# Kernel tuning notes

Hardware: AMD Instinct MI355X
Metric: run time of the kernel (lower is better)

## Reference

```python
import jax, jax.numpy as jnp
import numpy as np

N_VAR = 1_000_000
N_CON = 500_000
N_EDGE = 8_000_000
H = 10  # n_h_feats


def setup_inputs() -> dict:
    key = jax.random.key(0)
    ks = jax.random.split(key, 20)
    f32 = jnp.float32
    s = 0.3  # weight init scale
    return {
        'var_c': jax.random.normal(ks[0], (N_VAR,), f32),
        'var_x': jax.random.normal(ks[1], (N_VAR,), f32),
        'con_b': jax.random.normal(ks[2], (N_CON,), f32),
        'edge_src': jax.random.randint(ks[3], (N_EDGE,), 0, N_VAR, jnp.int32),
        'edge_dst': jax.random.randint(ks[4], (N_EDGE,), 0, N_CON, jnp.int32),
        'edge_w': jax.random.uniform(ks[5], (N_EDGE,), f32),
        'Wv': jax.random.normal(ks[6], (2, H), f32) * s,
        'bv': jnp.zeros((H,), f32),
        'Wc': jax.random.normal(ks[7], (1, H), f32) * s,
        'bc': jnp.zeros((H,), f32),
        'W1': jax.random.normal(ks[8], (H, H), f32) * s,
        'b1': jnp.zeros((H,), f32),
        'W2': jax.random.normal(ks[9], (H, H), f32) * s,
        'b2': jnp.zeros((H,), f32),
        'Wo1': jax.random.normal(ks[10], (H, H), f32) * s,
        'bo1': jnp.zeros((H,), f32),
        'Wo2': jax.random.normal(ks[11], (H, H), f32) * s,
        'bo2': jnp.zeros((H,), f32),
        'Wo3': jax.random.normal(ks[12], (H, 1), f32) * s,
        'bo3': jnp.zeros((1,), f32),
    }


def _graph_conv(feat_src, src, dst, w, n_dst, deg_src, deg_dst, W, b):
    # DGL GraphConv, norm='both', with edge weights:
    # h = D_src^{-1/2} x ; m_e = h[src_e] * w_e ; agg = scatter_sum(m, dst)
    # out = (D_dst^{-1/2} agg) @ W + b
    h = feat_src * jax.lax.rsqrt(deg_src)[:, None]
    m = h[src] * w[:, None]                      # [E, H] gather + scale
    agg = jax.ops.segment_sum(m, dst, num_segments=n_dst)  # scatter-add
    agg = agg * jax.lax.rsqrt(deg_dst)[:, None]
    return agg @ W + b


def reference(var_c, var_x, con_b, edge_src, edge_dst, edge_w,
              Wv, bv, Wc, bc, W1, b1, W2, b2, Wo1, bo1, Wo2, bo2, Wo3, bo3):
    # node embeddings
    var_feat = jnp.stack([var_c, var_x], axis=1)            # [N_VAR, 2]
    con_feat = con_b.reshape(-1, 1)                          # [N_CON, 1]
    X_var = jax.nn.relu(var_feat @ Wv + bv)                  # [N_VAR, H]
    X_con = jax.nn.relu(con_feat @ Wc + bc)                  # computed in original; unused by GraphConv (no dst-feat term)

    ones_e = jnp.ones((edge_src.shape[0],), jnp.float32)
    deg_var = jnp.maximum(jax.ops.segment_sum(ones_e, edge_src, num_segments=N_VAR), 1.0)
    deg_con = jnp.maximum(jax.ops.segment_sum(ones_e, edge_dst, num_segments=N_CON), 1.0)

    # conv1['con'] is overwritten by conv2['con'] in the original (v2c src feats are X_var both times)
    h_con = jax.nn.relu(_graph_conv(X_var, edge_src, edge_dst, edge_w, N_CON, deg_var, deg_con, W2, b2))
    # likewise conv1['var'] is overwritten by conv2['var'] (c2v src feats are h_con both times)
    h_var = jax.nn.relu(_graph_conv(h_con, edge_dst, edge_src, edge_w, N_VAR, deg_con, deg_var, W2, b2))

    z = jax.nn.relu(h_var @ Wo1 + bo1)
    z = jax.nn.relu(z @ Wo2 + bo2)
    logit = z @ Wo3 + bo3                                    # [N_VAR, 1]
    # dgl.readout_nodes(op='mean') over a single batched graph
    return jnp.mean(logit, axis=0, keepdims=True)            # [1, 1]
```

## Files before the change

kernel.cpp:

```cpp
#include <hip/hip_runtime.h>

#define NVAR 1000000
#define NCON 500000
#define EPB 8192
#define FCAP 4480


__global__ __launch_bounds__(256) void kA_hist2(const int4* __restrict__ src4,
                                                const int4* __restrict__ dst4,
                                                unsigned* __restrict__ bhV,
                                                unsigned* __restrict__ bhC,
                                                int ne4, int nblk) {
    __shared__ unsigned hv[1024], hc[1024];
    int tid = threadIdx.x, b = blockIdx.x;
    for (int t = tid; t < 1024; t += 256) { hv[t] = 0; hc[t] = 0; }
    __syncthreads();
    int beg = b * (EPB / 4), end = min(ne4, beg + (EPB / 4));
    for (int i = beg + tid; i < end; i += 256) {
        int4 s = src4[i];
        int4 d = dst4[i];
        atomicAdd(&hv[s.x >> 10], 1u); atomicAdd(&hv[s.y >> 10], 1u);
        atomicAdd(&hv[s.z >> 10], 1u); atomicAdd(&hv[s.w >> 10], 1u);
        atomicAdd(&hc[d.x >> 9], 1u);  atomicAdd(&hc[d.y >> 9], 1u);
        atomicAdd(&hc[d.z >> 9], 1u);  atomicAdd(&hc[d.w >> 9], 1u);
    }
    __syncthreads();
    for (int t = tid; t < 1024; t += 256) {
        bhV[(size_t)t * nblk + b] = hv[t];
        bhC[(size_t)t * nblk + b] = hc[t];
    }
}

__global__ __launch_bounds__(256) void kA_scat(const int* __restrict__ keys,
                                               const int* __restrict__ vals,
                                               const float* __restrict__ w,
                                               const unsigned int* __restrict__ scanned,
                                               int2* __restrict__ bucketed,
                                               int ne, int shift, int nblk) {
    __shared__ unsigned int h[1024];
    __shared__ unsigned int lb[1024];
    __shared__ unsigned int gb[1024];
    __shared__ unsigned int sc[256];
    __shared__ int2 stage[EPB];
    __shared__ unsigned short sbkt[EPB];
    int tid = threadIdx.x, b = blockIdx.x;
    for (int t = tid; t < 1024; t += 256) {
        h[t] = 0;
        gb[t] = scanned[(size_t)t * nblk + b];
    }
    __syncthreads();
    int beg = b * EPB, end = min(ne, beg + EPB), cnt = end - beg;
    int cnt4 = cnt >> 2;
    const int4* keys4 = (const int4*)(keys + beg);
    for (int i = tid; i < cnt4; i += 256) {
        int4 k = keys4[i];
        atomicAdd(&h[k.x >> shift], 1u);
        atomicAdd(&h[k.y >> shift], 1u);
        atomicAdd(&h[k.z >> shift], 1u);
        atomicAdd(&h[k.w >> shift], 1u);
    }
    for (int i = cnt4 * 4 + tid; i < cnt; i += 256) atomicAdd(&h[keys[beg + i] >> shift], 1u);
    __syncthreads();
    unsigned v0, v1, v2, v3;
    int q = tid * 4;
    v0 = h[q]; v1 = h[q + 1]; v2 = h[q + 2]; v3 = h[q + 3];
    sc[tid] = v0 + v1 + v2 + v3;
    __syncthreads();
    for (int dd = 1; dd < 256; dd <<= 1) {
        unsigned add = (tid >= dd) ? sc[tid - dd] : 0u;
        __syncthreads();
        sc[tid] += add;
        __syncthreads();
    }
    unsigned ex = (tid == 0) ? 0u : sc[tid - 1];
    lb[q]     = ex;
    lb[q + 1] = ex + v0;
    lb[q + 2] = ex + v0 + v1;
    lb[q + 3] = ex + v0 + v1 + v2;
    __syncthreads();
    for (int t = tid; t < 1024; t += 256) h[t] = 0;
    __syncthreads();
    unsigned mask = (1u << shift) - 1u;
    const int4* vals4 = (const int4*)(vals + beg);
    const float4* w4 = (const float4*)(w + beg);
    for (int i = tid; i < cnt4; i += 256) {
        int4 k = keys4[i];
        int4 v = vals4[i];
        float4 ww = w4[i];
        {
            unsigned bkt = (unsigned)k.x >> shift;
            unsigned r = atomicAdd(&h[bkt], 1u);
            unsigned slot = lb[bkt] + r;
            stage[slot] = make_int2(__float_as_int(ww.x),
                                    (v.x << shift) | (unsigned)(k.x & (int)mask));
            sbkt[slot] = (unsigned short)bkt;
        }
        {
            unsigned bkt = (unsigned)k.y >> shift;
            unsigned r = atomicAdd(&h[bkt], 1u);
            unsigned slot = lb[bkt] + r;
            stage[slot] = make_int2(__float_as_int(ww.y),
                                    (v.y << shift) | (unsigned)(k.y & (int)mask));
            sbkt[slot] = (unsigned short)bkt;
        }
        {
            unsigned bkt = (unsigned)k.z >> shift;
            unsigned r = atomicAdd(&h[bkt], 1u);
            unsigned slot = lb[bkt] + r;
            stage[slot] = make_int2(__float_as_int(ww.z),
                                    (v.z << shift) | (unsigned)(k.z & (int)mask));
            sbkt[slot] = (unsigned short)bkt;
        }
        {
            unsigned bkt = (unsigned)k.w >> shift;
            unsigned r = atomicAdd(&h[bkt], 1u);
            unsigned slot = lb[bkt] + r;
            stage[slot] = make_int2(__float_as_int(ww.w),
                                    (v.w << shift) | (unsigned)(k.w & (int)mask));
            sbkt[slot] = (unsigned short)bkt;
        }
    }
    for (int i = cnt4 * 4 + tid; i < cnt; i += 256) {
        int k = keys[beg + i];
        unsigned bkt = (unsigned)k >> shift;
        unsigned r = atomicAdd(&h[bkt], 1u);
        unsigned slot = lb[bkt] + r;
        stage[slot] = make_int2(__float_as_int(w[beg + i]),
                                (vals[beg + i] << shift) | (unsigned)(k & (int)mask));
        sbkt[slot] = (unsigned short)bkt;
    }
    __syncthreads();
    for (int i = tid; i < cnt; i += 256) {
        unsigned bb = sbkt[i];
        bucketed[gb[bb] + ((unsigned)i - lb[bb])] = stage[i];
    }
}

__global__ __launch_bounds__(256) void kDeg(const int2* __restrict__ bucketed,
                                            const unsigned* __restrict__ scanned,
                                            unsigned* __restrict__ deg,
                                            int nnodes, int nblk, int lowbits) {
    __shared__ unsigned h[1024];
    int d = blockIdx.x, tid = threadIdx.x;
    int W = 1 << lowbits;
    unsigned mask = (unsigned)(W - 1);
    unsigned base = scanned[(size_t)d * nblk], next = scanned[(size_t)(d + 1) * nblk];
    for (int t = tid; t < W; t += 256) h[t] = 0;
    __syncthreads();
    for (unsigned i = base + tid; i < next; i += 256)
        atomicAdd(&h[(unsigned)bucketed[i].y & mask], 1u);
    __syncthreads();
    int lo = d << lowbits;
    for (int t = tid; t < W; t += 256) {
        int node = lo + t;
        if (node < nnodes) deg[node] = h[t];
    }
}

__global__ __launch_bounds__(256) void kDegPackV(const int2* __restrict__ bucketed,
                                                 const unsigned* __restrict__ scanned,
                                                 const float* __restrict__ var_c,
                                                 const float* __restrict__ var_x,
                                                 unsigned* __restrict__ deg,
                                                 float4* __restrict__ vcr,
                                                 int nnodes, int nblk) {
    __shared__ unsigned h[1024];
    int d = blockIdx.x, tid = threadIdx.x;
    unsigned base = scanned[(size_t)d * nblk], next = scanned[(size_t)(d + 1) * nblk];
    for (int t = tid; t < 1024; t += 256) h[t] = 0;
    __syncthreads();
    for (unsigned i = base + tid; i < next; i += 256)
        atomicAdd(&h[(unsigned)bucketed[i].y & 1023u], 1u);
    __syncthreads();
    int lo = d << 10;
    for (int t = tid; t < 1024; t += 256) {
        int node = lo + t;
        if (node < nnodes) {
            unsigned dg = h[t];
            deg[node] = dg;
            float rs = rsqrtf(fmaxf((float)dg, 1.0f));
            vcr[node] = make_float4(var_c[node], var_x[node], rs, 0.0f);
        }
    }
}

__global__ __launch_bounds__(256) void k_scan_blocks(const unsigned int* in,
                                                     unsigned int* out,
                                                     unsigned int* bsum,
                                                     int n) {
    __shared__ unsigned int sT[256];
    int base = blockIdx.x * 1024 + threadIdx.x * 4;
    unsigned int v0 = 0, v1 = 0, v2 = 0, v3 = 0;
    if (base + 3 < n) {
        uint4 u = *(const uint4*)(in + base);
        v0 = u.x; v1 = u.y; v2 = u.z; v3 = u.w;
    } else {
        if (base     < n) v0 = in[base];
        if (base + 1 < n) v1 = in[base + 1];
        if (base + 2 < n) v2 = in[base + 2];
        if (base + 3 < n) v3 = in[base + 3];
    }
    sT[threadIdx.x] = v0 + v1 + v2 + v3;
    __syncthreads();
    for (int d = 1; d < 256; d <<= 1) {
        unsigned int add = (threadIdx.x >= (unsigned)d) ? sT[threadIdx.x - d] : 0u;
        __syncthreads();
        sT[threadIdx.x] += add;
        __syncthreads();
    }
    unsigned int excl = (threadIdx.x == 0) ? 0u : sT[threadIdx.x - 1];
    if (base     < n) out[base]     = excl;
    if (base + 1 < n) out[base + 1] = excl + v0;
    if (base + 2 < n) out[base + 2] = excl + v0 + v1;
    if (base + 3 < n) out[base + 3] = excl + v0 + v1 + v2;
    if (threadIdx.x == 255 && bsum) bsum[blockIdx.x] = sT[255];
}

__global__ __launch_bounds__(256) void k_scan_mid(const unsigned* __restrict__ in,
                                                  unsigned* __restrict__ out, int n) {
    __shared__ unsigned sT[256];
    __shared__ unsigned carry;
    if (threadIdx.x == 0) carry = 0;
    __syncthreads();
    for (int base = 0; base < n; base += 256) {
        int i = base + threadIdx.x;
        unsigned v = (i < n) ? in[i] : 0u;
        sT[threadIdx.x] = v;
        __syncthreads();
        for (int d = 1; d < 256; d <<= 1) {
            unsigned add = (threadIdx.x >= (unsigned)d) ? sT[threadIdx.x - d] : 0u;
            __syncthreads();
            sT[threadIdx.x] += add;
            __syncthreads();
        }
        unsigned excl = carry + ((threadIdx.x == 0) ? 0u : sT[threadIdx.x - 1]);
        if (i < n) out[i] = excl;
        __syncthreads();
        if (threadIdx.x == 255) carry += sT[255];
        __syncthreads();
    }
}

__global__ __launch_bounds__(256) void k_scan_add(unsigned int* __restrict__ data,
                                                  const unsigned int* __restrict__ bscan,
                                                  int n) {
    int base = blockIdx.x * 1024 + threadIdx.x * 4;
    unsigned int add = bscan[blockIdx.x];
    if (base + 3 < n) {
        uint4 u = *(const uint4*)(data + base);
        u.x += add; u.y += add; u.z += add; u.w += add;
        *(uint4*)(data + base) = u;
    } else {
        if (base     < n) data[base]     += add;
        if (base + 1 < n) data[base + 1] += add;
        if (base + 2 < n) data[base + 2] += add;
        if (base + 3 < n) data[base + 3] += add;
    }
}


#define EMBADD(e)                                                             \
    {                                                                         \
        float4 vv = vcr[(size_t)(e).y];                                       \
        float we = __int_as_float((e).x);                                     \
        float t0 = fmaf(vv.x, wv0[0], fmaf(vv.y, wv1[0], bvr[0]));            \
        float t1 = fmaf(vv.x, wv0[1], fmaf(vv.y, wv1[1], bvr[1]));            \
        float t2 = fmaf(vv.x, wv0[2], fmaf(vv.y, wv1[2], bvr[2]));            \
        float t3 = fmaf(vv.x, wv0[3], fmaf(vv.y, wv1[3], bvr[3]));            \
        acc.x = fmaf(we, fmaxf(t0, 0.f) * vv.z, acc.x);                       \
        acc.y = fmaf(we, fmaxf(t1, 0.f) * vv.z, acc.y);                       \
        acc.z = fmaf(we, fmaxf(t2, 0.f) * vv.z, acc.z);                       \
        acc.w = fmaf(we, fmaxf(t3, 0.f) * vv.z, acc.w);                       \
    }

#define EMB4(eA, eB, eC, eD)                                                  \
    {                                                                         \
        float4 vA = vcr[(size_t)(eA).y];                                      \
        float4 vB = vcr[(size_t)(eB).y];                                      \
        float4 vC = vcr[(size_t)(eC).y];                                      \
        float4 vD = vcr[(size_t)(eD).y];                                      \
        float wA = __int_as_float((eA).x), wB = __int_as_float((eB).x);       \
        float wC = __int_as_float((eC).x), wD = __int_as_float((eD).x);       \
        float t0, t1, t2, t3;                                                 \
        t0 = fmaf(vA.x, wv0[0], fmaf(vA.y, wv1[0], bvr[0]));                  \
        t1 = fmaf(vA.x, wv0[1], fmaf(vA.y, wv1[1], bvr[1]));                  \
        t2 = fmaf(vA.x, wv0[2], fmaf(vA.y, wv1[2], bvr[2]));                  \
        t3 = fmaf(vA.x, wv0[3], fmaf(vA.y, wv1[3], bvr[3]));                  \
        acc.x = fmaf(wA, fmaxf(t0, 0.f) * vA.z, acc.x);                       \
        acc.y = fmaf(wA, fmaxf(t1, 0.f) * vA.z, acc.y);                       \
        acc.z = fmaf(wA, fmaxf(t2, 0.f) * vA.z, acc.z);                       \
        acc.w = fmaf(wA, fmaxf(t3, 0.f) * vA.z, acc.w);                       \
        t0 = fmaf(vB.x, wv0[0], fmaf(vB.y, wv1[0], bvr[0]));                  \
        t1 = fmaf(vB.x, wv0[1], fmaf(vB.y, wv1[1], bvr[1]));                  \
        t2 = fmaf(vB.x, wv0[2], fmaf(vB.y, wv1[2], bvr[2]));                  \
        t3 = fmaf(vB.x, wv0[3], fmaf(vB.y, wv1[3], bvr[3]));                  \
        acc.x = fmaf(wB, fmaxf(t0, 0.f) * vB.z, acc.x);                       \
        acc.y = fmaf(wB, fmaxf(t1, 0.f) * vB.z, acc.y);                       \
        acc.z = fmaf(wB, fmaxf(t2, 0.f) * vB.z, acc.z);                       \
        acc.w = fmaf(wB, fmaxf(t3, 0.f) * vB.z, acc.w);                       \
        t0 = fmaf(vC.x, wv0[0], fmaf(vC.y, wv1[0], bvr[0]));                  \
        t1 = fmaf(vC.x, wv0[1], fmaf(vC.y, wv1[1], bvr[1]));                  \
        t2 = fmaf(vC.x, wv0[2], fmaf(vC.y, wv1[2], bvr[2]));                  \
        t3 = fmaf(vC.x, wv0[3], fmaf(vC.y, wv1[3], bvr[3]));                  \
        acc.x = fmaf(wC, fmaxf(t0, 0.f) * vC.z, acc.x);                       \
        acc.y = fmaf(wC, fmaxf(t1, 0.f) * vC.z, acc.y);                       \
        acc.z = fmaf(wC, fmaxf(t2, 0.f) * vC.z, acc.z);                       \
        acc.w = fmaf(wC, fmaxf(t3, 0.f) * vC.z, acc.w);                       \
        t0 = fmaf(vD.x, wv0[0], fmaf(vD.y, wv1[0], bvr[0]));                  \
        t1 = fmaf(vD.x, wv0[1], fmaf(vD.y, wv1[1], bvr[1]));                  \
        t2 = fmaf(vD.x, wv0[2], fmaf(vD.y, wv1[2], bvr[2]));                  \
        t3 = fmaf(vD.x, wv0[3], fmaf(vD.y, wv1[3], bvr[3]));                  \
        acc.x = fmaf(wD, fmaxf(t0, 0.f) * vD.z, acc.x);                       \
        acc.y = fmaf(wD, fmaxf(t1, 0.f) * vD.z, acc.y);                       \
        acc.z = fmaf(wD, fmaxf(t2, 0.f) * vD.z, acc.z);                       \
        acc.w = fmaf(wD, fmaxf(t3, 0.f) * vD.z, acc.w);                       \
    }

__global__ __launch_bounds__(512) void kF_con(const int2* __restrict__ bucketed,
                                              const unsigned* __restrict__ scanned,
                                              const unsigned* __restrict__ startC,
                                              const float4* __restrict__ vcr,
                                              const float* __restrict__ Wv,
                                              const float* __restrict__ bv,
                                              const float* __restrict__ W2,
                                              const float* __restrict__ b2,
                                              float* __restrict__ hs, int nblk, int netot) {
    __shared__ unsigned sraw[257], cr[256];
    __shared__ float sWv[20], sbv[10], sW[100], sb[10];
    __shared__ int2 stage[FCAP];
    int tid = threadIdx.x;
    int d = blockIdx.x >> 1, half = blockIdx.x & 1;
    int gbase = (d << 9) + half * 256;
    for (int t = tid; t < 100; t += 512) sW[t] = W2[t];
    if (tid < 10) sb[tid] = b2[tid];
    if (tid < 20) sWv[tid] = Wv[tid];
    if (tid >= 20 && tid < 30) sbv[tid - 20] = bv[tid - 20];
    for (int t = tid; t < 257; t += 512) {
        int g = gbase + t;
        sraw[t] = (g < NCON) ? startC[g] : (unsigned)netot;
    }
    if (tid < 256) cr[tid] = 0;
    __syncthreads();
    unsigned own_beg = sraw[0], own_end = sraw[256];
    bool fit = (int)(own_end - own_beg) <= FCAP;
    unsigned bbase = scanned[(size_t)d * nblk];
    unsigned bnext = scanned[(size_t)(d + 1) * nblk];
    int bsz = (int)(bnext - bbase);
    if (fit) {
        for (int i = tid; i < bsz; i += 512) {
            int2 p = bucketed[bbase + i];
            unsigned low = (unsigned)p.y & 511u;
            if ((int)(low >> 8) == half) {
                unsigned nl = low & 255u;
                unsigned r = atomicAdd(&cr[nl], 1u);
                stage[sraw[nl] - own_beg + r] = make_int2(p.x, p.y >> 9);
            }
        }
    }
    __syncthreads();
    int quad = tid >> 2, lane = tid & 3, c0 = lane * 4;
    float wv0[4], wv1[4], bvr[4];
#pragma unroll
    for (int k = 0; k < 4; k++) {
        int j = c0 + k;
        wv0[k] = (j < 10) ? sWv[j] : 0.f;
        wv1[k] = (j < 10) ? sWv[10 + j] : 0.f;
        bvr[k] = (j < 10) ? sbv[j] : 0.f;
    }
#pragma unroll
    for (int rr = 0; rr < 2; rr++) {
        int nl = rr * 128 + quad;
        int g = gbase + nl;
        if (g >= NCON) continue;
        float4 acc = make_float4(0.f, 0.f, 0.f, 0.f);
        unsigned cnt;
        if (fit) {
            unsigned beg = sraw[nl] - own_beg;
            cnt = cr[nl];
            unsigned end = beg + cnt, p = beg;
            for (; p + 4 <= end; p += 4) {
                int2 e0 = stage[p], e1 = stage[p + 1], e2 = stage[p + 2], e3 = stage[p + 3];
                EMB4(e0, e1, e2, e3);
            }
            for (; p < end; ++p) {
                int2 e = stage[p];
                EMBADD(e);
            }
        } else {
            cnt = 0;
            unsigned target = (unsigned)(half * 256 + nl);
            for (int i = 0; i < bsz; ++i) {
                int2 p = bucketed[bbase + i];
                if (((unsigned)p.y & 511u) == target) {
                    ++cnt;
                    int2 e = make_int2(p.x, p.y >> 9);
                    EMBADD(e);
                }
            }
        }
        float rs = rsqrtf(fmaxf((float)cnt, 1.0f));
        float a[10];
        a[0] = __shfl(acc.x, 0, 4); a[1] = __shfl(acc.y, 0, 4);
        a[2] = __shfl(acc.z, 0, 4); a[3] = __shfl(acc.w, 0, 4);
        a[4] = __shfl(acc.x, 1, 4); a[5] = __shfl(acc.y, 1, 4);
        a[6] = __shfl(acc.z, 1, 4); a[7] = __shfl(acc.w, 1, 4);
        a[8] = __shfl(acc.x, 2, 4); a[9] = __shfl(acc.y, 2, 4);
#pragma unroll
        for (int j = 0; j < 10; j++) a[j] *= rs;
        float o[12];
#pragma unroll
        for (int k = 0; k < 10; k++) {
            float t = sb[k];
#pragma unroll
            for (int j = 0; j < 10; j++) t = fmaf(a[j], sW[j * 10 + k], t);
            o[k] = fmaxf(t, 0.0f) * rs;
        }
        o[10] = 0.0f; o[11] = 0.0f;
        float4 wv = (lane < 3) ? make_float4(o[c0], o[c0 + 1], o[c0 + 2], o[c0 + 3])
                               : make_float4(0.f, 0.f, 0.f, 0.f);
        *(float4*)(hs + (size_t)g * 16 + c0) = wv;
    }
}

#define GATHER4(eA, eB, eC, eD, TAB)                                          \
    {                                                                         \
        float4 v0 = *(const float4*)(TAB + (size_t)(eA).y * 16 + c0);         \
        float4 v1 = *(const float4*)(TAB + (size_t)(eB).y * 16 + c0);         \
        float4 v2 = *(const float4*)(TAB + (size_t)(eC).y * 16 + c0);         \
        float4 v3 = *(const float4*)(TAB + (size_t)(eD).y * 16 + c0);         \
        float w0 = __int_as_float((eA).x), w1 = __int_as_float((eB).x);       \
        float w2 = __int_as_float((eC).x), w3 = __int_as_float((eD).x);       \
        acc.x = fmaf(w0, v0.x, acc.x); acc.y = fmaf(w0, v0.y, acc.y);         \
        acc.z = fmaf(w0, v0.z, acc.z); acc.w = fmaf(w0, v0.w, acc.w);         \
        acc.x = fmaf(w1, v1.x, acc.x); acc.y = fmaf(w1, v1.y, acc.y);         \
        acc.z = fmaf(w1, v1.z, acc.z); acc.w = fmaf(w1, v1.w, acc.w);         \
        acc.x = fmaf(w2, v2.x, acc.x); acc.y = fmaf(w2, v2.y, acc.y);         \
        acc.z = fmaf(w2, v2.z, acc.z); acc.w = fmaf(w2, v2.w, acc.w);         \
        acc.x = fmaf(w3, v3.x, acc.x); acc.y = fmaf(w3, v3.y, acc.y);         \
        acc.z = fmaf(w3, v3.z, acc.z); acc.w = fmaf(w3, v3.w, acc.w);         \
    }

__global__ __launch_bounds__(512) void kF_fin(const int2* __restrict__ bucketed,
                                              const unsigned* __restrict__ scanned,
                                              const unsigned* __restrict__ startV,
                                              const float* __restrict__ feat,
                                              const float* __restrict__ W2,
                                              const float* __restrict__ b2,
                                              const float* __restrict__ Wo1,
                                              const float* __restrict__ bo1,
                                              const float* __restrict__ Wo2,
                                              const float* __restrict__ bo2,
                                              const float* __restrict__ Wo3,
                                              const float* __restrict__ bo3,
                                              double* __restrict__ partials, int nblk, int netot) {
    __shared__ unsigned sraw[513], cr[512];
    __shared__ float sW2[100], sb2[10], sWo1[100], sbo1[10], sWo2[100], sbo2[10], sWo3[10], sbo3v;
    __shared__ int2 stage[FCAP];
    __shared__ double red[512];
    int tid = threadIdx.x;
    int d = blockIdx.x >> 1, half = blockIdx.x & 1;
    int gbase = (d << 10) + half * 512;
    for (int t = tid; t < 100; t += 512) { sW2[t] = W2[t]; sWo1[t] = Wo1[t]; sWo2[t] = Wo2[t]; }
    if (tid < 10) {
        sb2[tid] = b2[tid]; sbo1[tid] = bo1[tid]; sbo2[tid] = bo2[tid]; sWo3[tid] = Wo3[tid];
    }
    if (tid == 0) sbo3v = bo3[0];
    for (int t = tid; t < 513; t += 512) {
        int g = gbase + t;
        sraw[t] = (g < NVAR) ? startV[g] : (unsigned)netot;
    }
    cr[tid] = 0;
    __syncthreads();
    unsigned own_beg = sraw[0], own_end = sraw[512];
    bool fit = (int)(own_end - own_beg) <= FCAP;
    unsigned bbase = scanned[(size_t)d * nblk];
    unsigned bnext = scanned[(size_t)(d + 1) * nblk];
    int bsz = (int)(bnext - bbase);
    if (fit) {
        for (int i = tid; i < bsz; i += 512) {
            int2 p = bucketed[bbase + i];
            unsigned low = (unsigned)p.y & 1023u;
            if ((int)(low >> 9) == half) {
                unsigned nl = low & 511u;
                unsigned r = atomicAdd(&cr[nl], 1u);
                stage[sraw[nl] - own_beg + r] = make_int2(p.x, p.y >> 10);
            }
        }
    }
    __syncthreads();
    int quad = tid >> 2, lane = tid & 3, c0 = lane * 4;
    double accd = 0.0;
#pragma unroll
    for (int rr = 0; rr < 4; rr++) {
        int nl = rr * 128 + quad;
        int g = gbase + nl;
        if (g >= NVAR) continue;
        float4 acc = make_float4(0.f, 0.f, 0.f, 0.f);
        unsigned cnt;
        if (fit) {
            unsigned beg = sraw[nl] - own_beg;
            cnt = cr[nl];
            unsigned end = beg + cnt, p = beg;
            for (; p + 4 <= end; p += 4) {
                int2 e0 = stage[p], e1 = stage[p + 1], e2 = stage[p + 2], e3 = stage[p + 3];
                GATHER4(e0, e1, e2, e3, feat);
            }
            for (; p < end; ++p) {
                int2 e = stage[p];
                float4 v = *(const float4*)(feat + (size_t)e.y * 16 + c0);
                float we = __int_as_float(e.x);
                acc.x = fmaf(we, v.x, acc.x); acc.y = fmaf(we, v.y, acc.y);
                acc.z = fmaf(we, v.z, acc.z); acc.w = fmaf(we, v.w, acc.w);
            }
        } else {
            cnt = 0;
            unsigned target = (unsigned)(half * 512 + nl);
            for (int i = 0; i < bsz; ++i) {
                int2 p = bucketed[bbase + i];
                if (((unsigned)p.y & 1023u) == target) {
                    ++cnt;
                    float4 v = *(const float4*)(feat + (size_t)((unsigned)p.y >> 10) * 16 + c0);
                    float we = __int_as_float(p.x);
                    acc.x = fmaf(we, v.x, acc.x); acc.y = fmaf(we, v.y, acc.y);
                    acc.z = fmaf(we, v.z, acc.z); acc.w = fmaf(we, v.w, acc.w);
                }
            }
        }
        float rs = rsqrtf(fmaxf((float)cnt, 1.0f));
        float a[10];
        a[0] = __shfl(acc.x, 0, 4); a[1] = __shfl(acc.y, 0, 4);
        a[2] = __shfl(acc.z, 0, 4); a[3] = __shfl(acc.w, 0, 4);
        a[4] = __shfl(acc.x, 1, 4); a[5] = __shfl(acc.y, 1, 4);
        a[6] = __shfl(acc.z, 1, 4); a[7] = __shfl(acc.w, 1, 4);
        a[8] = __shfl(acc.x, 2, 4); a[9] = __shfl(acc.y, 2, 4);
#pragma unroll
        for (int j = 0; j < 10; j++) a[j] *= rs;
        float hh[10], z[10];
#pragma unroll
        for (int k = 0; k < 10; k++) {
            float t = sb2[k];
#pragma unroll
            for (int j = 0; j < 10; j++) t = fmaf(a[j], sW2[j * 10 + k], t);
            hh[k] = fmaxf(t, 0.0f);
        }
#pragma unroll
        for (int k = 0; k < 10; k++) {
            float t = sbo1[k];
#pragma unroll
            for (int j = 0; j < 10; j++) t = fmaf(hh[j], sWo1[j * 10 + k], t);
            z[k] = fmaxf(t, 0.0f);
        }
        float t3 = sbo3v;
#pragma unroll
        for (int k = 0; k < 10; k++) {
            float t = sbo2[k];
#pragma unroll
            for (int j = 0; j < 10; j++) t = fmaf(z[j], sWo2[j * 10 + k], t);
            t = fmaxf(t, 0.0f);
            t3 = fmaf(t, sWo3[k], t3);
        }
        if (lane == 0) accd += (double)t3;
    }
    red[tid] = accd;
    __syncthreads();
    for (int off = 256; off > 0; off >>= 1) {
        if (tid < off) red[tid] += red[tid + off];
        __syncthreads();
    }
    if (tid == 0) partials[blockIdx.x] = red[0];
}

__global__ __launch_bounds__(256) void k_out(const double* __restrict__ partials, int np,
                                             float* __restrict__ out) {
    __shared__ double red[256];
    double a = 0.0;
    for (int i = threadIdx.x; i < np; i += blockDim.x) a += partials[i];
    red[threadIdx.x] = a;
    __syncthreads();
    for (int off = 128; off > 0; off >>= 1) {
        if (threadIdx.x < off) red[threadIdx.x] += red[threadIdx.x + off];
        __syncthreads();
    }
    if (threadIdx.x == 0) out[0] = (float)(red[0] / (double)NVAR);
}


extern "C" void kernel_launch(void* const* d_in, const int* in_sizes, int n_in,
                              void* d_out, int out_size, void* d_ws, size_t ws_size,
                              hipStream_t stream) {
    const float* var_c  = (const float*)d_in[0];
    const float* var_x  = (const float*)d_in[1];
    const int*   e_src  = (const int*)d_in[3];
    const int*   e_dst  = (const int*)d_in[4];
    const float* e_w    = (const float*)d_in[5];
    const float* Wv     = (const float*)d_in[6];
    const float* bv     = (const float*)d_in[7];
    const float* W2     = (const float*)d_in[12];
    const float* b2     = (const float*)d_in[13];
    const float* Wo1    = (const float*)d_in[14];
    const float* bo1    = (const float*)d_in[15];
    const float* Wo2    = (const float*)d_in[16];
    const float* bo2    = (const float*)d_in[17];
    const float* Wo3    = (const float*)d_in[18];
    const float* bo3    = (const float*)d_in[19];
    float* out = (float*)d_out;
    const int ne = in_sizes[3];
    (void)n_in; (void)out_size; (void)ws_size;

    const int B = 256;
    const int nblkA = (ne + EPB - 1) / EPB;
    const int scanN = 1024 * nblkA;
    const int NBs   = (scanN + 1023) / 1024;
    const int BKV   = (NVAR + 1023) >> 10;
    const int BKC   = (NCON + 511) >> 9;
    const int NBV   = (NVAR + 1023) / 1024;
    const int NBC   = (NCON + 1023) / 1024;
    const int ne4   = ne / 4;

    char* ws = (char*)d_ws;
    size_t off = 0;
    auto walloc = [&](size_t bytes) {
        void* p = ws + off;
        off = (off + bytes + 255) & ~(size_t)255;
        return p;
    };

    int2*     bucketedV = (int2*)walloc((size_t)ne * 8);
    int2*     bucketedC = (int2*)walloc((size_t)ne * 8);
    float4*   vcr       = (float4*)walloc((size_t)NVAR * 16);
    float*    hs64      = (float*)walloc((size_t)NCON * 16 * 4);
    unsigned* scannedV  = (unsigned*)walloc((size_t)scanN * 4);
    unsigned* scannedC  = (unsigned*)walloc((size_t)scanN * 4);
    unsigned* bhV       = (unsigned*)walloc((size_t)scanN * 4);
    unsigned* bhC       = (unsigned*)walloc((size_t)scanN * 4);
    unsigned* bsumA     = (unsigned*)walloc(8192);
    unsigned* bscanA    = (unsigned*)walloc(8192);
    double*   partials  = (double*)walloc((size_t)(BKV * 2) * 8 + 64);
    unsigned* deg_var   = bhV;
    unsigned* deg_con   = bhC;

    kA_hist2<<<nblkA, B, 0, stream>>>((const int4*)e_src, (const int4*)e_dst,
                                      bhV, bhC, ne4, nblkA);

    k_scan_blocks<<<NBs, B, 0, stream>>>(bhV, scannedV, bsumA, scanN);
    k_scan_mid   <<<1,   B, 0, stream>>>(bsumA, bscanA, NBs);
    k_scan_add   <<<NBs, B, 0, stream>>>(scannedV, bscanA, scanN);
    k_scan_blocks<<<NBs, B, 0, stream>>>(bhC, scannedC, bsumA, scanN);
    k_scan_mid   <<<1,   B, 0, stream>>>(bsumA, bscanA, NBs);
    k_scan_add   <<<NBs, B, 0, stream>>>(scannedC, bscanA, scanN);

    kA_scat<<<nblkA, B, 0, stream>>>(e_src, e_dst, e_w, scannedV, bucketedV, ne, 10, nblkA);

    kDegPackV<<<BKV, B, 0, stream>>>(bucketedV, scannedV, var_c, var_x,
                                     deg_var, vcr, NVAR, nblkA);

    k_scan_blocks<<<NBV, B, 0, stream>>>(deg_var, deg_var, bsumA, NVAR);
    k_scan_mid   <<<1,   B, 0, stream>>>(bsumA, bscanA, NBV);
    k_scan_add   <<<NBV, B, 0, stream>>>(deg_var, bscanA, NVAR);

    kA_scat<<<nblkA, B, 0, stream>>>(e_dst, e_src, e_w, scannedC, bucketedC, ne, 9, nblkA);

    kDeg<<<BKC, B, 0, stream>>>(bucketedC, scannedC, deg_con, NCON, nblkA, 9);
    k_scan_blocks<<<NBC, B, 0, stream>>>(deg_con, deg_con, bsumA, NCON);
    k_scan_mid   <<<1,   B, 0, stream>>>(bsumA, bscanA, NBC);
    k_scan_add   <<<NBC, B, 0, stream>>>(deg_con, bscanA, NCON);

    kF_con<<<BKC * 2, 512, 0, stream>>>(bucketedC, scannedC, deg_con, vcr, Wv, bv,
                                        W2, b2, hs64, nblkA, ne);

    kF_fin<<<BKV * 2, 512, 0, stream>>>(bucketedV, scannedV, deg_var, hs64, W2, b2,
                                        Wo1, bo1, Wo2, bo2, Wo3, bo3, partials, nblkA, ne);

    k_out<<<1, B, 0, stream>>>(partials, BKV * 2, out);
}
```

Baseline: 564.3 us.

## Reuse per-block histograms in scatter and transpose histogram layout

The histogram kernel now writes per-block bucket counts row-major and two transpose kernels produce the column-major layout the scans need. The scatter kernel loads its block's histogram instead of recomputing it with shared atomics over the keys. It also drops the per-slot bucket array, finding each slot's bucket by binary search over the local offsets. This removes a key re-read and an atomic pass per scatter and cuts shared memory, at the cost of two extra launches, some extra global traffic and search work in the write-out loop.

```diff
diff --git a/kernel.cpp b/kernel.cpp
--- a/kernel.cpp
+++ b/kernel.cpp
@@ -8,9 +8,9 @@
 
 __global__ __launch_bounds__(256) void kA_hist2(const int4* __restrict__ src4,
                                                 const int4* __restrict__ dst4,
-                                                unsigned* __restrict__ bhV,
-                                                unsigned* __restrict__ bhC,
-                                                int ne4, int nblk) {
+                                                unsigned* __restrict__ bhTV,
+                                                unsigned* __restrict__ bhTC,
+                                                int ne4) {
     __shared__ unsigned hv[1024], hc[1024];
     int tid = threadIdx.x, b = blockIdx.x;
     for (int t = tid; t < 1024; t += 256) { hv[t] = 0; hc[t] = 0; }
@@ -26,14 +26,33 @@
     }
     __syncthreads();
     for (int t = tid; t < 1024; t += 256) {
-        bhV[(size_t)t * nblk + b] = hv[t];
-        bhC[(size_t)t * nblk + b] = hc[t];
+        bhTV[(size_t)b * 1024 + t] = hv[t];
+        bhTC[(size_t)b * 1024 + t] = hc[t];
+    }
+}
+
+__global__ __launch_bounds__(256) void k_transpose(const unsigned* __restrict__ in,
+                                                   unsigned* __restrict__ out, int R) {
+    __shared__ unsigned tile[32][33];
+    int ct = blockIdx.x, rt = blockIdx.y;
+    int tx = threadIdx.x & 31, ty = threadIdx.x >> 5;
+#pragma unroll
+    for (int k = 0; k < 4; k++) {
+        int r = rt * 32 + ty + k * 8, c = ct * 32 + tx;
+        tile[ty + k * 8][tx] = (r < R) ? in[(size_t)r * 1024 + c] : 0u;
+    }
+    __syncthreads();
+#pragma unroll
+    for (int k = 0; k < 4; k++) {
+        int r2 = rt * 32 + tx, c2 = ct * 32 + ty + k * 8;
+        if (r2 < R) out[(size_t)c2 * R + r2] = tile[tx][ty + k * 8];
     }
 }
 
 __global__ __launch_bounds__(256) void kA_scat(const int* __restrict__ keys,
                                                const int* __restrict__ vals,
                                                const float* __restrict__ w,
+                                               const unsigned* __restrict__ bhT,
                                                const unsigned int* __restrict__ scanned,
                                                int2* __restrict__ bucketed,
                                                int ne, int shift, int nblk) {
@@ -42,25 +61,13 @@
     __shared__ unsigned int gb[1024];
     __shared__ unsigned int sc[256];
     __shared__ int2 stage[EPB];
-    __shared__ unsigned short sbkt[EPB];
     int tid = threadIdx.x, b = blockIdx.x;
     for (int t = tid; t < 1024; t += 256) {
-        h[t] = 0;
+        h[t] = bhT[(size_t)b * 1024 + t];
         gb[t] = scanned[(size_t)t * nblk + b];
     }
     __syncthreads();
     int beg = b * EPB, end = min(ne, beg + EPB), cnt = end - beg;
-    int cnt4 = cnt >> 2;
-    const int4* keys4 = (const int4*)(keys + beg);
-    for (int i = tid; i < cnt4; i += 256) {
-        int4 k = keys4[i];
-        atomicAdd(&h[k.x >> shift], 1u);
-        atomicAdd(&h[k.y >> shift], 1u);
-        atomicAdd(&h[k.z >> shift], 1u);
-        atomicAdd(&h[k.w >> shift], 1u);
-    }
-    for (int i = cnt4 * 4 + tid; i < cnt; i += 256) atomicAdd(&h[keys[beg + i] >> shift], 1u);
-    __syncthreads();
     unsigned v0, v1, v2, v3;
     int q = tid * 4;
     v0 = h[q]; v1 = h[q + 1]; v2 = h[q + 2]; v3 = h[q + 3];
@@ -81,6 +88,8 @@
     for (int t = tid; t < 1024; t += 256) h[t] = 0;
     __syncthreads();
     unsigned mask = (1u << shift) - 1u;
+    int cnt4 = cnt >> 2;
+    const int4* keys4 = (const int4*)(keys + beg);
     const int4* vals4 = (const int4*)(vals + beg);
     const float4* w4 = (const float4*)(w + beg);
     for (int i = tid; i < cnt4; i += 256) {
@@ -90,48 +99,43 @@
         {
             unsigned bkt = (unsigned)k.x >> shift;
             unsigned r = atomicAdd(&h[bkt], 1u);
-            unsigned slot = lb[bkt] + r;
-            stage[slot] = make_int2(__float_as_int(ww.x),
-                                    (v.x << shift) | (unsigned)(k.x & (int)mask));
-            sbkt[slot] = (unsigned short)bkt;
+            stage[lb[bkt] + r] = make_int2(__float_as_int(ww.x),
+                                           (v.x << shift) | (unsigned)(k.x & (int)mask));
         }
         {
             unsigned bkt = (unsigned)k.y >> shift;
             unsigned r = atomicAdd(&h[bkt], 1u);
-            unsigned slot = lb[bkt] + r;
-            stage[slot] = make_int2(__float_as_int(ww.y),
-                                    (v.y << shift) | (unsigned)(k.y & (int)mask));
-            sbkt[slot] = (unsigned short)bkt;
+            stage[lb[bkt] + r] = make_int2(__float_as_int(ww.y),
+                                           (v.y << shift) | (unsigned)(k.y & (int)mask));
         }
         {
             unsigned bkt = (unsigned)k.z >> shift;
             unsigned r = atomicAdd(&h[bkt], 1u);
-            unsigned slot = lb[bkt] + r;
-            stage[slot] = make_int2(__float_as_int(ww.z),
-                                    (v.z << shift) | (unsigned)(k.z & (int)mask));
-            sbkt[slot] = (unsigned short)bkt;
+            stage[lb[bkt] + r] = make_int2(__float_as_int(ww.z),
+                                           (v.z << shift) | (unsigned)(k.z & (int)mask));
         }
         {
             unsigned bkt = (unsigned)k.w >> shift;
             unsigned r = atomicAdd(&h[bkt], 1u);
-            unsigned slot = lb[bkt] + r;
-            stage[slot] = make_int2(__float_as_int(ww.w),
-                                    (v.w << shift) | (unsigned)(k.w & (int)mask));
-            sbkt[slot] = (unsigned short)bkt;
+            stage[lb[bkt] + r] = make_int2(__float_as_int(ww.w),
+                                           (v.w << shift) | (unsigned)(k.w & (int)mask));
         }
     }
     for (int i = cnt4 * 4 + tid; i < cnt; i += 256) {
         int k = keys[beg + i];
         unsigned bkt = (unsigned)k >> shift;
         unsigned r = atomicAdd(&h[bkt], 1u);
-        unsigned slot = lb[bkt] + r;
-        stage[slot] = make_int2(__float_as_int(w[beg + i]),
-                                (vals[beg + i] << shift) | (unsigned)(k & (int)mask));
-        sbkt[slot] = (unsigned short)bkt;
+        stage[lb[bkt] + r] = make_int2(__float_as_int(w[beg + i]),
+                                       (vals[beg + i] << shift) | (unsigned)(k & (int)mask));
     }
     __syncthreads();
     for (int i = tid; i < cnt; i += 256) {
-        unsigned bb = sbkt[i];
+        unsigned bb = 0;
+#pragma unroll
+        for (int step = 512; step > 0; step >>= 1) {
+            unsigned cand = bb + step;
+            if (cand < 1024 && lb[cand] <= (unsigned)i) bb = cand;
+        }
         bucketed[gb[bb] + ((unsigned)i - lb[bb])] = stage[i];
     }
 }
@@ -633,6 +637,8 @@
     unsigned* scannedC  = (unsigned*)walloc((size_t)scanN * 4);
     unsigned* bhV       = (unsigned*)walloc((size_t)scanN * 4);
     unsigned* bhC       = (unsigned*)walloc((size_t)scanN * 4);
+    unsigned* bhTV      = (unsigned*)walloc((size_t)scanN * 4);
+    unsigned* bhTC      = (unsigned*)walloc((size_t)scanN * 4);
     unsigned* bsumA     = (unsigned*)walloc(8192);
     unsigned* bscanA    = (unsigned*)walloc(8192);
     double*   partials  = (double*)walloc((size_t)(BKV * 2) * 8 + 64);
@@ -640,7 +646,11 @@
     unsigned* deg_con   = bhC;
 
     kA_hist2<<<nblkA, B, 0, stream>>>((const int4*)e_src, (const int4*)e_dst,
-                                      bhV, bhC, ne4, nblkA);
+                                      bhTV, bhTC, ne4);
+
+    dim3 tgrid(1024 / 32, (nblkA + 31) / 32);
+    k_transpose<<<tgrid, B, 0, stream>>>(bhTV, bhV, nblkA);
+    k_transpose<<<tgrid, B, 0, stream>>>(bhTC, bhC, nblkA);
 
     k_scan_blocks<<<NBs, B, 0, stream>>>(bhV, scannedV, bsumA, scanN);
     k_scan_mid   <<<1,   B, 0, stream>>>(bsumA, bscanA, NBs);
@@ -649,7 +659,8 @@
     k_scan_mid   <<<1,   B, 0, stream>>>(bsumA, bscanA, NBs);
     k_scan_add   <<<NBs, B, 0, stream>>>(scannedC, bscanA, scanN);
 
-    kA_scat<<<nblkA, B, 0, stream>>>(e_src, e_dst, e_w, scannedV, bucketedV, ne, 10, nblkA);
+    kA_scat<<<nblkA, B, 0, stream>>>(e_src, e_dst, e_w, bhTV, scannedV, bucketedV,
+                                     ne, 10, nblkA);
 
     kDegPackV<<<BKV, B, 0, stream>>>(bucketedV, scannedV, var_c, var_x,
                                      deg_var, vcr, NVAR, nblkA);
@@ -658,7 +669,8 @@
     k_scan_mid   <<<1,   B, 0, stream>>>(bsumA, bscanA, NBV);
     k_scan_add   <<<NBV, B, 0, stream>>>(deg_var, bscanA, NVAR);
 
-    kA_scat<<<nblkA, B, 0, stream>>>(e_dst, e_src, e_w, scannedC, bucketedC, ne, 9, nblkA);
+    kA_scat<<<nblkA, B, 0, stream>>>(e_dst, e_src, e_w, bhTC, scannedC, bucketedC,
+                                     ne, 9, nblkA);
 
     kDeg<<<BKC, B, 0, stream>>>(bucketedC, scannedC, deg_con, NCON, nblkA, 9);
     k_scan_blocks<<<NBC, B, 0, stream>>>(deg_con, deg_con, bsumA, NCON);
```

Result: faster. 526.1 us (-6.8%).
